# Optimization experiments

Hardware: AMD Instinct MI355X
Metric: run time of the kernel (lower is better)

Reference implementation:

```python
import jax, jax.numpy as jnp
import numpy as np

D_MODEL = 1024
D_INNER = 1024          # expand=1
NQK = 32
NV = 32
DSTATE = 64
DCONV = 4
CHUNK = 128
CONV_DIM = D_INNER + 2 * NQK * DSTATE          # 5120
HEADDIM = D_INNER // NV                         # 32
IN_PROJ_OUT = 2 * D_INNER + 2 * NQK * DSTATE + NV  # 6176


def setup_inputs() -> dict:
    key = jax.random.key(0)
    ks = jax.random.split(key, 6)
    B, L = 2, 8192
    u = jax.random.normal(ks[0], (B, L, D_MODEL), jnp.float32)
    W_in = jax.random.normal(ks[1], (IN_PROJ_OUT, D_MODEL), jnp.float32) * 0.02
    conv_w = jax.random.normal(ks[2], (CONV_DIM, DCONV), jnp.float32) * 0.2
    conv_b = jax.random.normal(ks[3], (CONV_DIM,), jnp.float32) * 0.02
    z_bias = jnp.zeros((D_INNER,), jnp.float32)
    D = jnp.ones((NV,), jnp.float32)
    W_out = jax.random.normal(ks[4], (D_MODEL, D_INNER), jnp.float32) * 0.02
    return {"u": u, "W_in": W_in, "conv_w": conv_w, "conv_b": conv_b,
            "z_bias": z_bias, "D": D, "W_out": W_out}


def _segsum(x):
    # x: (b,h,c,l) -> (b,h,c,l,l); entry (i,j) = sum_{j<s<=i} x_s for i>=j, masked else
    l = x.shape[-1]
    cs = jnp.cumsum(x, -1)
    seg = cs[..., :, None] - cs[..., None, :]
    mask = jnp.tril(jnp.ones((l, l), bool))
    return jnp.where(mask, seg, -1e9)


def reference(u, W_in, conv_w, conv_b, z_bias, D, W_out):
    b, L, _ = u.shape
    # in_proj and split: xBC | z | A_log
    xBCzA = u @ W_in.T
    xBC = xBCzA[..., :CONV_DIM]
    z = xBCzA[..., CONV_DIM:CONV_DIM + D_INNER]
    A_log = xBCzA[..., CONV_DIM + D_INNER:]          # (b,L,NV)
    # causal depthwise conv1d, identity activation
    xp = jnp.pad(xBC, ((0, 0), (DCONV - 1, 0), (0, 0)))
    xBC = sum(conv_w[:, k] * xp[:, k:k + L, :] for k in range(DCONV)) + conv_b
    # split x, B, C and reshape to heads
    x = xBC[..., :D_INNER].reshape(b, L, NV, HEADDIM)
    Bm = xBC[..., D_INNER:D_INNER + NQK * DSTATE].reshape(b, L, NQK, DSTATE)
    Cm = xBC[..., D_INNER + NQK * DSTATE:].reshape(b, L, NQK, DSTATE)
    # dt = softplus(A_log); A = -1 per head; kernel uses (x/dt) and multiplies dt back in
    dt = jax.nn.softplus(A_log)                      # (b,L,h)
    x_sc = x / dt[..., None]
    Xdt = x_sc * dt[..., None]
    Adt = -dt
    # chunked SSD (mamba_chunk_scan_combined math)
    nc = L // CHUNK
    Ac = Adt.reshape(b, nc, CHUNK, NV).transpose(0, 3, 1, 2)   # (b,h,c,l)
    A_cum = jnp.cumsum(Ac, -1)
    Lmat = jnp.exp(_segsum(Ac))                                # (b,h,c,l,l)
    Bc = Bm.reshape(b, nc, CHUNK, NQK, DSTATE)
    Cc = Cm.reshape(b, nc, CHUNK, NQK, DSTATE)
    Xc = Xdt.reshape(b, nc, CHUNK, NV, HEADDIM)
    # intra-chunk (diagonal block) output
    Y_diag = jnp.einsum('bclhn,bcshn,bhcls,bcshp->bclhp', Cc, Bc, Lmat, Xc)
    # per-chunk final states
    decay_states = jnp.exp(A_cum[..., -1:] - A_cum)            # (b,h,c,l)
    states = jnp.einsum('bclhn,bhcl,bclhp->bchpn', Bc, decay_states, Xc)
    dc = jnp.exp(A_cum[..., -1])                               # (b,h,c)
    st = jnp.moveaxis(states, 1, 0)                            # (c,b,h,p,n)
    dcs = jnp.moveaxis(dc, 2, 0)                               # (c,b,h)

    def step(S, inp):
        s_c, d_c = inp
        prev = S
        S = S * d_c[..., None, None] + s_c
        return S, prev

    S0 = jnp.zeros((b, NV, HEADDIM, DSTATE), Xdt.dtype)
    _, prevs = jax.lax.scan(step, S0, (st, dcs))               # (c,b,h,p,n)
    prevs = jnp.moveaxis(prevs, 0, 1)                          # (b,c,h,p,n)
    # inter-chunk (off-diagonal) contribution
    Y_off = jnp.einsum('bclhn,bchpn,bhcl->bclhp', Cc, prevs, jnp.exp(A_cum))
    y = (Y_diag + Y_off).reshape(b, L, NV, HEADDIM)
    # skip connection uses the UNscaled x (per torch code)
    y = y + D[None, None, :, None] * x
    y = y.reshape(b, L, D_INNER)
    # gated output projection
    return (y * jax.nn.silu(z + z_bias)) @ W_out.T
```

## Files before the change

### kernel.cpp

```cpp
#include <hip/hip_runtime.h>

typedef unsigned short u16;
typedef unsigned int   u32;
typedef __bf16  bf16x8 __attribute__((ext_vector_type(8)));
typedef float   f32x4  __attribute__((ext_vector_type(4)));
typedef unsigned int u32x4 __attribute__((ext_vector_type(4)));
typedef unsigned int u32x2 __attribute__((ext_vector_type(2)));

__device__ __forceinline__ float bf2f(u16 h){ return __uint_as_float(((u32)h)<<16); }
__device__ __forceinline__ u16 f2bf(float f){
  u32 u = __float_as_uint(f);
  u += 0x7FFFu + ((u>>16)&1u);
  return (u16)(u>>16);
}
__device__ __forceinline__ f32x4 mfma16(bf16x8 a, bf16x8 b, f32x4 c){
  return __builtin_amdgcn_mfma_f32_16x16x32_bf16(a,b,c,0,0,0);
}
__device__ __forceinline__ void ld16_lds(const u16* g, u16* l){
  __builtin_amdgcn_global_load_lds((const __attribute__((address_space(1))) u32*)g,
                                   (__attribute__((address_space(3))) u32*)l, 16, 0, 0);
}

__global__ __launch_bounds__(256) void cvt_kernel(const float* __restrict__ in,
                                                  u16* __restrict__ out, int n4){
  int i = blockIdx.x*256 + threadIdx.x;
  if (i < n4){
    float4 v = ((const float4*)in)[i];
    u32 p0 = (u32)f2bf(v.x) | ((u32)f2bf(v.y)<<16);
    u32 p1 = (u32)f2bf(v.z) | ((u32)f2bf(v.w)<<16);
    u32x2 pv = {p0, p1};
    *(u32x2*)(out + (size_t)i*4) = pv;
  }
}

__global__ __launch_bounds__(256) void dt_kernel(const float* __restrict__ u,
                                                 const float* __restrict__ Win,
                                                 float* __restrict__ dtb){
  __shared__ float us[8][1028];
  const int tid = threadIdx.x;
  const size_t t0 = (size_t)blockIdx.x*8;
  for (int i=tid; i<2048; i+=256){
    int row = i>>8, col = (i&255)*4;
    *(float4*)&us[row][col] = *(const float4*)(u + (t0+row)*1024 + col);
  }
  __syncthreads();
  const int tok = tid & 7, h = tid >> 3;
  const float* wp = Win + (size_t)(6144+h)*1024;
  float s0=0.f,s1=0.f,s2=0.f,s3=0.f;
  for (int k=0;k<1024;k+=4){
    float4 a  = *(const float4*)&us[tok][k];
    float4 wv = *(const float4*)&wp[k];
    s0 += a.x*wv.x; s1 += a.y*wv.y; s2 += a.z*wv.z; s3 += a.w*wv.w;
  }
  float s = (s0+s1)+(s2+s3);
  dtb[(t0+tok)*32 + h] = (s > 15.f) ? s : log1pf(expf(s));
}

__global__ __launch_bounds__(256,2) void gemm_in(const u16* __restrict__ A,
                                                 const u16* __restrict__ Bw,
                                                 u16* __restrict__ out0,
                                                 u16* __restrict__ out1,
                                                 const float* __restrict__ zb){
  __shared__ u16 As[128*32];
  __shared__ u16 Bs[128*32];
  const int tid  = threadIdx.x;
  const int lane = tid & 63;
  const int w = tid >> 6, wm = w >> 1, wn = w & 1;
  const int quad = lane >> 4, l15 = lane & 15;

  const int hwid = (int)(blockIdx.y*48 + blockIdx.x);
  const int tile = (hwid & 7)*384 + (hwid >> 3);
  const size_t m0 = (size_t)(tile / 48)*128, n0 = (size_t)(tile % 48)*128;

  f32x4 acc[4][4];
  #pragma unroll
  for (int i=0;i<4;i++)
    #pragma unroll
    for (int j=0;j<4;j++){ f32x4 z = {0.f,0.f,0.f,0.f}; acc[i][j] = z; }

  const int srow    = w*16 + (lane>>2);
  const int scol_sw = ((lane&3) ^ ((lane>>3)&3))*8;
  const u16* gA = A  + (m0+srow)*1024 + scol_sw;
  const u16* gB = Bw + (n0+srow)*1024 + scol_sw;
  u16* lA = As + w*512;
  u16* lB = Bs + w*512;

  const int swz = (quad*8) ^ (((l15>>1)&3)<<3);

  for (int k0 = 0; k0 < 1024; k0 += 32){
    __syncthreads();
    ld16_lds(gA,          lA);
    ld16_lds(gA + 64*1024, lA + 2048);
    ld16_lds(gB,          lB);
    ld16_lds(gB + 64*1024, lB + 2048);
    gA += 32; gB += 32;
    __syncthreads();
    bf16x8 av[4], bv[4];
    #pragma unroll
    for (int mi=0;mi<4;mi++) av[mi] = *(const bf16x8*)&As[(wm*64+mi*16+l15)*32 + swz];
    #pragma unroll
    for (int ni=0;ni<4;ni++) bv[ni] = *(const bf16x8*)&Bs[(wn*64+ni*16+l15)*32 + swz];
    #pragma unroll
    for (int mi=0;mi<4;mi++)
      #pragma unroll
      for (int ni=0;ni<4;ni++)
        acc[mi][ni] = mfma16(av[mi], bv[ni], acc[mi][ni]);
  }

  #pragma unroll
  for (int mi=0;mi<4;mi++){
    #pragma unroll
    for (int ni=0;ni<4;ni++){
      #pragma unroll
      for (int r=0;r<4;r++){
        size_t row = m0 + wm*64 + mi*16 + quad*4 + r;
        int    col = (int)n0 + wn*64 + ni*16 + l15;
        float v = acc[mi][ni][r];
        if (col < 5120){
          out0[row*5120 + col] = f2bf(v);
        } else {
          int ch = col - 5120;
          float z = v + zb[ch];
          float sg = z / (1.f + __expf(-z));
          out1[row*1024 + ch] = f2bf(sg);
        }
      }
    }
  }
}

__global__ __launch_bounds__(256,2) void gemm_out(const u16* __restrict__ A,
                                                  const u16* __restrict__ Bw,
                                                  float* __restrict__ out0){
  __shared__ u16 As[128*32];
  __shared__ u16 Bs[128*32];
  const int tid  = threadIdx.x;
  const int lane = tid & 63;
  const int w = tid >> 6, wm = w >> 1, wn = w & 1;
  const int quad = lane >> 4, l15 = lane & 15;

  const int hwid = (int)(blockIdx.y*8 + blockIdx.x);
  const int tile = (hwid & 7)*64 + (hwid >> 3);
  const size_t m0 = (size_t)(tile / 8)*128, n0 = (size_t)(tile % 8)*128;

  f32x4 acc[4][4];
  #pragma unroll
  for (int i=0;i<4;i++)
    #pragma unroll
    for (int j=0;j<4;j++){ f32x4 z = {0.f,0.f,0.f,0.f}; acc[i][j] = z; }

  const int srow    = w*16 + (lane>>2);
  const int scol_sw = ((lane&3) ^ ((lane>>3)&3))*8;
  const u16* gA = A  + (m0+srow)*1024 + scol_sw;
  const u16* gB = Bw + (n0+srow)*1024 + scol_sw;
  u16* lA = As + w*512;
  u16* lB = Bs + w*512;

  const int swz = (quad*8) ^ (((l15>>1)&3)<<3);

  for (int k0 = 0; k0 < 1024; k0 += 32){
    __syncthreads();
    ld16_lds(gA,          lA);
    ld16_lds(gA + 64*1024, lA + 2048);
    ld16_lds(gB,          lB);
    ld16_lds(gB + 64*1024, lB + 2048);
    gA += 32; gB += 32;
    __syncthreads();
    bf16x8 av[4], bv[4];
    #pragma unroll
    for (int mi=0;mi<4;mi++) av[mi] = *(const bf16x8*)&As[(wm*64+mi*16+l15)*32 + swz];
    #pragma unroll
    for (int ni=0;ni<4;ni++) bv[ni] = *(const bf16x8*)&Bs[(wn*64+ni*16+l15)*32 + swz];
    #pragma unroll
    for (int mi=0;mi<4;mi++)
      #pragma unroll
      for (int ni=0;ni<4;ni++)
        acc[mi][ni] = mfma16(av[mi], bv[ni], acc[mi][ni]);
  }

  #pragma unroll
  for (int mi=0;mi<4;mi++)
    #pragma unroll
    for (int ni=0;ni<4;ni++)
      #pragma unroll
      for (int r=0;r<4;r++){
        size_t row = m0 + wm*64 + mi*16 + quad*4 + r;
        int    col = (int)n0 + wn*64 + ni*16 + l15;
        out0[row*1024 + col] = acc[mi][ni][r];
      }
}

__global__ __launch_bounds__(256) void conv_kernel(const u16* __restrict__ xraw,
                                                   const float* __restrict__ cw,
                                                   const float* __restrict__ cb,
                                                   u16* __restrict__ xconv){
  const int c  = blockIdx.x*256 + threadIdx.x;
  const int t0 = blockIdx.y*8;
  const float w0=cw[c*4+0], w1=cw[c*4+1], w2=cw[c*4+2], w3=cw[c*4+3], bias=cb[c];
  const size_t base = (size_t)c;
  float h0 = (t0>=3) ? bf2f(xraw[base + (size_t)(t0-3)*5120]) : 0.f;
  float h1 = (t0>=2) ? bf2f(xraw[base + (size_t)(t0-2)*5120]) : 0.f;
  float h2 = (t0>=1) ? bf2f(xraw[base + (size_t)(t0-1)*5120]) : 0.f;
  #pragma unroll
  for (int i=0;i<8;i++){
    float x = bf2f(xraw[base + (size_t)(t0+i)*5120]);
    float o = w0*h0 + w1*h1 + w2*h2 + w3*x + bias;
    xconv[base + (size_t)(t0+i)*5120] = f2bf(o);
    h0=h1; h1=h2; h2=x;
  }
}

__global__ __launch_bounds__(256,1) void chunk1_kernel(const u16* __restrict__ xconv,
                                                       const float* __restrict__ dtb,
                                                       const float* __restrict__ Dvec,
                                                       float* __restrict__ ypart,
                                                       float* __restrict__ states,
                                                       float* __restrict__ dcb){
  __shared__ u16 Ps[128*136];
  __shared__ u16 XT[32*136];
  __shared__ u16 BT[64*136];
  __shared__ float Acum[128];
  __shared__ float decay[128];

  const int tid = threadIdx.x;
  const int lane = tid & 63;
  const int w = tid >> 6, quad = lane >> 4, l15 = lane & 15;
  const int blk = blockIdx.x;
  const int h = blk & 31, c = blk >> 5;
  const size_t tok0 = (size_t)c*128;
  const size_t xbase = tok0 * 5120;

  float mdt = 0.f;
  if (tid < 128) mdt = -dtb[(tok0 + tid)*32 + h];

  #pragma unroll
  for (int p=0;p<2;p++){
    int idx = p*256 + tid;
    int row = idx >> 2, col = (idx & 3)*8;
    u32x4 v = *(const u32x4*)(xconv + xbase + (size_t)row*5120 + h*32 + col);
    const u16* pv = (const u16*)&v;
    #pragma unroll
    for (int j=0;j<8;j++) XT[(col+j)*136 + row] = pv[j];
  }
  #pragma unroll
  for (int p=0;p<4;p++){
    int idx = p*256 + tid;
    int row = idx >> 3, col = (idx & 7)*8;
    u32x4 v = *(const u32x4*)(xconv + xbase + (size_t)row*5120 + 1024 + h*64 + col);
    const u16* pv = (const u16*)&v;
    #pragma unroll
    for (int j=0;j<8;j++) BT[(col+j)*136 + row] = pv[j];
  }
  if (tid < 128) Acum[tid] = mdt;
  __syncthreads();
  float run = mdt;
  for (int off=1; off<128; off<<=1){
    float add = 0.f;
    if (tid < 128 && tid >= off) add = Acum[tid-off];
    __syncthreads();
    if (tid < 128){ run += add; Acum[tid] = run; }
    __syncthreads();
  }
  float Alast = Acum[127];
  if (tid < 128) decay[tid] = __expf(Alast - Acum[tid]);
  if (tid == 0)  dcb[blk] = __expf(Alast);

  const int wm = w >> 1, wn = w & 1;
  f32x4 g[4][4];
  #pragma unroll
  for (int i=0;i<4;i++)
    #pragma unroll
    for (int j=0;j<4;j++){ f32x4 z = {0.f,0.f,0.f,0.f}; g[i][j] = z; }
  #pragma unroll
  for (int kk=0; kk<2; kk++){
    bf16x8 av[4], bv[4];
    #pragma unroll
    for (int mi=0;mi<4;mi++){
      int row = wm*64 + mi*16 + l15;
      av[mi] = *(const bf16x8*)(xconv + xbase + (size_t)row*5120 + 3072 + h*64 + kk*32 + quad*8);
    }
    #pragma unroll
    for (int ni=0;ni<4;ni++){
      int row = wn*64 + ni*16 + l15;
      bv[ni] = *(const bf16x8*)(xconv + xbase + (size_t)row*5120 + 1024 + h*64 + kk*32 + quad*8);
    }
    #pragma unroll
    for (int mi=0;mi<4;mi++)
      #pragma unroll
      for (int ni=0;ni<4;ni++)
        g[mi][ni] = mfma16(av[mi], bv[ni], g[mi][ni]);
  }
  #pragma unroll
  for (int mi=0;mi<4;mi++){
    int rowb = wm*64 + mi*16 + quad*4;
    #pragma unroll
    for (int ni=0;ni<4;ni++){
      int col = wn*64 + ni*16 + l15;
      float ac = Acum[col];
      #pragma unroll
      for (int r=0;r<4;r++){
        int row = rowb + r;
        float val = 0.f;
        if (col <= row) val = g[mi][ni][r] * __expf(Acum[row] - ac);
        Ps[row*136 + col] = f2bf(val);
      }
    }
  }
  __syncthreads();

  f32x4 yd[2][2];
  #pragma unroll
  for (int i=0;i<2;i++)
    #pragma unroll
    for (int j=0;j<2;j++){ f32x4 z = {0.f,0.f,0.f,0.f}; yd[i][j] = z; }
  #pragma unroll
  for (int kk=0;kk<4;kk++){
    bf16x8 av[2], bv[2];
    #pragma unroll
    for (int mi=0;mi<2;mi++) av[mi] = *(const bf16x8*)&Ps[(w*32+mi*16+l15)*136 + kk*32 + quad*8];
    #pragma unroll
    for (int ni=0;ni<2;ni++) bv[ni] = *(const bf16x8*)&XT[(ni*16+l15)*136 + kk*32 + quad*8];
    #pragma unroll
    for (int mi=0;mi<2;mi++)
      #pragma unroll
      for (int ni=0;ni<2;ni++)
        yd[mi][ni] = mfma16(av[mi], bv[ni], yd[mi][ni]);
  }
  float Dh = Dvec[h];
  #pragma unroll
  for (int mi=0;mi<2;mi++)
    #pragma unroll
    for (int ni=0;ni<2;ni++)
      #pragma unroll
      for (int r=0;r<4;r++){
        int row = w*32 + mi*16 + quad*4 + r;
        int col = ni*16 + l15;
        float xval = bf2f(XT[col*136 + row]);
        ypart[(tok0+row)*1024 + h*32 + col] = yd[mi][ni][r] + Dh*xval;
      }

  const int wm2 = w >> 1, wn2 = w & 1;
  f32x4 st[2];
  { f32x4 z = {0.f,0.f,0.f,0.f}; st[0]=z; st[1]=z; }
  #pragma unroll
  for (int kk=0;kk<4;kk++){
    bf16x8 av;
    {
      u32x4 xv = *(const u32x4*)&XT[(wm2*16+l15)*136 + kk*32 + quad*8];
      const u16* xp = (const u16*)&xv;
      #pragma unroll
      for (int j=0;j<8;j++) ((__bf16*)&av)[j] = (__bf16)(bf2f(xp[j]) * decay[kk*32 + quad*8 + j]);
    }
    bf16x8 bv[2];
    #pragma unroll
    for (int ni=0;ni<2;ni++) bv[ni] = *(const bf16x8*)&BT[(wn2*32+ni*16+l15)*136 + kk*32 + quad*8];
    #pragma unroll
    for (int ni=0;ni<2;ni++) st[ni] = mfma16(av, bv[ni], st[ni]);
  }
  size_t sbase = (size_t)blk * 2048;
  #pragma unroll
  for (int ni=0;ni<2;ni++)
    #pragma unroll
    for (int r=0;r<4;r++){
      int row = wm2*16 + quad*4 + r;
      int col = wn2*32 + ni*16 + l15;
      states[sbase + row*64 + col] = st[ni][r];
    }
}

__global__ __launch_bounds__(256) void scan_kernel(float* __restrict__ states,
                                                   const float* __restrict__ dcb){
  const int h = blockIdx.x >> 3;
  const int part = blockIdx.x & 7;
  const int pn = part*256 + threadIdx.x;
  float r[64];
  #pragma unroll
  for (int c=0;c<64;c++) r[c] = states[((size_t)(c*32 + h))*2048 + pn];
  float S = 0.f;
  #pragma unroll
  for (int c=0;c<64;c++){
    float stv = r[c];
    states[((size_t)(c*32 + h))*2048 + pn] = S;
    S = S*dcb[c*32 + h] + stv;
  }
}

__global__ __launch_bounds__(256,1) void chunk3_kernel(const u16* __restrict__ xconv,
                                                       const float* __restrict__ dtb,
                                                       const float* __restrict__ prevs,
                                                       const float* __restrict__ ypart,
                                                       const u16* __restrict__ gate,
                                                       u16* __restrict__ yg){
  __shared__ u16 Pv[32*72];
  __shared__ float Acum[128];
  const int tid = threadIdx.x;
  const int lane = tid & 63;
  const int w = tid >> 6, quad = lane >> 4, l15 = lane & 15;
  const int blk = blockIdx.x;
  const int h = blk & 31, c = blk >> 5;
  const size_t tok0 = (size_t)c*128;
  const size_t xbase = tok0 * 5120;

  float mdt = 0.f;
  if (tid < 128) mdt = -dtb[(tok0 + tid)*32 + h];
  size_t sbase = (size_t)blk * 2048;
  #pragma unroll
  for (int p=0;p<8;p++){
    int i = p*256 + tid;
    int pp = i >> 6, nn = i & 63;
    Pv[pp*72 + nn] = f2bf(prevs[sbase + i]);
  }
  if (tid < 128) Acum[tid] = mdt;
  __syncthreads();
  float run = mdt;
  for (int off=1; off<128; off<<=1){
    float add = 0.f;
    if (tid < 128 && tid >= off) add = Acum[tid-off];
    __syncthreads();
    if (tid < 128){ run += add; Acum[tid] = run; }
    __syncthreads();
  }

  f32x4 yo[2][2];
  #pragma unroll
  for (int i=0;i<2;i++)
    #pragma unroll
    for (int j=0;j<2;j++){ f32x4 z = {0.f,0.f,0.f,0.f}; yo[i][j] = z; }
  #pragma unroll
  for (int kk=0;kk<2;kk++){
    bf16x8 av[2], bv[2];
    #pragma unroll
    for (int mi=0;mi<2;mi++){
      int row = w*32 + mi*16 + l15;
      av[mi] = *(const bf16x8*)(xconv + xbase + (size_t)row*5120 + 3072 + h*64 + kk*32 + quad*8);
    }
    #pragma unroll
    for (int ni=0;ni<2;ni++) bv[ni] = *(const bf16x8*)&Pv[(ni*16+l15)*72 + kk*32 + quad*8];
    #pragma unroll
    for (int mi=0;mi<2;mi++)
      #pragma unroll
      for (int ni=0;ni<2;ni++)
        yo[mi][ni] = mfma16(av[mi], bv[ni], yo[mi][ni]);
  }
  #pragma unroll
  for (int mi=0;mi<2;mi++)
    #pragma unroll
    for (int ni=0;ni<2;ni++)
      #pragma unroll
      for (int r=0;r<4;r++){
        int row = w*32 + mi*16 + quad*4 + r;
        int col = ni*16 + l15;
        size_t gi = (tok0+row)*1024 + h*32 + col;
        float val = (ypart[gi] + __expf(Acum[row]) * yo[mi][ni][r]) * bf2f(gate[gi]);
        yg[gi] = f2bf(val);
      }
}

extern "C" void kernel_launch(void* const* d_in, const int* in_sizes, int n_in,
                              void* d_out, int out_size, void* d_ws, size_t ws_size,
                              hipStream_t stream){
  (void)out_size; (void)ws_size;
  static const int want[7] = {16777216, 6324224, 20480, 5120, 1024, 32, 1048576};
  const void* src[7] = {nullptr,nullptr,nullptr,nullptr,nullptr,nullptr,nullptr};
  if (n_in >= 7){
    for (int i=0;i<7;i++)
      for (int j=0;j<n_in;j++)
        if (in_sizes[j] == want[i]){ src[i] = d_in[j]; break; }
  }
  bool ok = true;
  for (int i=0;i<7;i++) if (!src[i]) ok = false;
  if (!ok) for (int i=0;i<7;i++) src[i] = d_in[i];
  const float* u      = (const float*)src[0];
  const float* W_in   = (const float*)src[1];
  const float* conv_w = (const float*)src[2];
  const float* conv_b = (const float*)src[3];
  const float* z_bias = (const float*)src[4];
  const float* Dvec   = (const float*)src[5];
  const float* W_out  = (const float*)src[6];
  float* out = (float*)d_out;

  char* p = (char*)d_ws;
  u16* wi_bf   = (u16*)p;   p += (size_t)6144*1024*2;
  u16* wo_bf   = (u16*)p;   p += (size_t)1024*1024*2;
  u16* u_bf    = (u16*)p;   p += (size_t)16384*1024*2;
  float* dtb   = (float*)p; p += (size_t)16384*32*4;
  float* dcb   = (float*)p; p += (size_t)4096*4;
  u16* gate    = (u16*)p;   p += (size_t)8192*1024*2;
  u16* yg      = (u16*)p;   p += (size_t)8192*1024*2;
  char* xbcA   = p;         p += (size_t)8192*5120*2;
  u16* xconv   = (u16*)p;   p += (size_t)8192*5120*2;

  u16*   xbc_raw = (u16*)xbcA;
  float* ypart   = (float*)xbcA;
  float* states  = (float*)(xbcA + (size_t)8192*1024*4);

  cvt_kernel<<<16384, 256, 0, stream>>>(u,     u_bf,  16384*1024/4);
  cvt_kernel<<<6144,  256, 0, stream>>>(W_in,  wi_bf, 6144*1024/4);
  cvt_kernel<<<1024,  256, 0, stream>>>(W_out, wo_bf, 1024*1024/4);
  dt_kernel<<<2048, 256, 0, stream>>>(u, W_in, dtb);

  for (int b = 0; b < 2; b++){
    const u16* ub_bf = u_bf + (size_t)b*8192*1024;
    float*     dtb_b = dtb  + (size_t)b*8192*32;
    float*     dcb_b = dcb  + (size_t)b*2048;
    float*     out_b = out  + (size_t)b*8192*1024;
    gemm_in<<<dim3(48,64), 256, 0, stream>>>(ub_bf, wi_bf, xbc_raw, gate, z_bias);
    conv_kernel<<<dim3(20,1024), 256, 0, stream>>>(xbc_raw, conv_w, conv_b, xconv);
    chunk1_kernel<<<2048, 256, 0, stream>>>(xconv, dtb_b, Dvec, ypart, states, dcb_b);
    scan_kernel<<<256, 256, 0, stream>>>(states, dcb_b);
    chunk3_kernel<<<2048, 256, 0, stream>>>(xconv, dtb_b, states, ypart, gate, yg);
    gemm_out<<<dim3(8,64), 256, 0, stream>>>(yg, wo_bf, out_b);
  }
}
```

Measured before the change: 807.6 us.

## Double-buffer LDS with BK=64 in input/output projection GEMMs

Both projection GEMMs now use a BK=64 K-tile with two LDS buffers, so global-to-LDS loads for the next tile are issued while MFMAs consume the current one. This halves the number of K iterations and removes one of the two barriers per step. The XOR swizzle changes to match 64-element rows, and the grouped tile-ordering remap is dropped in favour of direct blockIdx mapping. LDS use per block grows fourfold to 64 KB, which may limit the two-blocks-per-CU occupancy, and dropping the remap may hurt L2 reuse.

```diff
diff --git a/kernel.cpp b/kernel.cpp
--- a/kernel.cpp
+++ b/kernel.cpp
@@ -61,16 +61,13 @@
                                                  u16* __restrict__ out0,
                                                  u16* __restrict__ out1,
                                                  const float* __restrict__ zb){
-  __shared__ u16 As[128*32];
-  __shared__ u16 Bs[128*32];
+  __shared__ u16 As[2*128*64];
+  __shared__ u16 Bs[2*128*64];
   const int tid  = threadIdx.x;
   const int lane = tid & 63;
   const int w = tid >> 6, wm = w >> 1, wn = w & 1;
   const int quad = lane >> 4, l15 = lane & 15;
-
-  const int hwid = (int)(blockIdx.y*48 + blockIdx.x);
-  const int tile = (hwid & 7)*384 + (hwid >> 3);
-  const size_t m0 = (size_t)(tile / 48)*128, n0 = (size_t)(tile % 48)*128;
+  const size_t m0 = (size_t)blockIdx.y*128, n0 = (size_t)blockIdx.x*128;
 
   f32x4 acc[4][4];
   #pragma unroll
@@ -78,34 +75,64 @@
     #pragma unroll
     for (int j=0;j<4;j++){ f32x4 z = {0.f,0.f,0.f,0.f}; acc[i][j] = z; }
 
-  const int srow    = w*16 + (lane>>2);
-  const int scol_sw = ((lane&3) ^ ((lane>>3)&3))*8;
+  const int srow    = w*32 + (lane>>3);
+  const int scol_sw = ((lane&7) ^ (lane>>3))*8;
   const u16* gA = A  + (m0+srow)*1024 + scol_sw;
   const u16* gB = Bw + (n0+srow)*1024 + scol_sw;
-  u16* lA = As + w*512;
-  u16* lB = Bs + w*512;
-
-  const int swz = (quad*8) ^ (((l15>>1)&3)<<3);
-
-  for (int k0 = 0; k0 < 1024; k0 += 32){
-    __syncthreads();
-    ld16_lds(gA,          lA);
-    ld16_lds(gA + 64*1024, lA + 2048);
-    ld16_lds(gB,          lB);
-    ld16_lds(gB + 64*1024, lB + 2048);
-    gA += 32; gB += 32;
-    __syncthreads();
-    bf16x8 av[4], bv[4];
-    #pragma unroll
-    for (int mi=0;mi<4;mi++) av[mi] = *(const bf16x8*)&As[(wm*64+mi*16+l15)*32 + swz];
-    #pragma unroll
-    for (int ni=0;ni<4;ni++) bv[ni] = *(const bf16x8*)&Bs[(wn*64+ni*16+l15)*32 + swz];
-    #pragma unroll
-    for (int mi=0;mi<4;mi++)
-      #pragma unroll
-      for (int ni=0;ni<4;ni++)
-        acc[mi][ni] = mfma16(av[mi], bv[ni], acc[mi][ni]);
-  }
+  const int lofs = w*2048;
+
+#define STG(BUF) do{                                   \
+    u16* la = As + (BUF)*8192 + lofs;                  \
+    u16* lb = Bs + (BUF)*8192 + lofs;                  \
+    ld16_lds(gA,         la);                          \
+    ld16_lds(gA +  8192, la + 512);                    \
+    ld16_lds(gA + 16384, la + 1024);                   \
+    ld16_lds(gA + 24576, la + 1536);                   \
+    ld16_lds(gB,         lb);                          \
+    ld16_lds(gB +  8192, lb + 512);                    \
+    ld16_lds(gB + 16384, lb + 1024);                   \
+    ld16_lds(gB + 24576, lb + 1536);                   \
+    gA += 64; gB += 64; }while(0)
+
+#define CMP(BUF) do{                                                            \
+    _Pragma("unroll")                                                           \
+    for (int kk=0;kk<2;kk++){                                                   \
+      bf16x8 av[4], bv[4];                                                      \
+      _Pragma("unroll")                                                         \
+      for (int mi=0;mi<4;mi++){                                                 \
+        int row = wm*64+mi*16+l15;                                              \
+        av[mi] = *(const bf16x8*)&As[(BUF)*8192 + row*64 + (((kk*4+quad) ^ (l15&7))*8)]; \
+      }                                                                         \
+      _Pragma("unroll")                                                         \
+      for (int ni=0;ni<4;ni++){                                                 \
+        int row = wn*64+ni*16+l15;                                              \
+        bv[ni] = *(const bf16x8*)&Bs[(BUF)*8192 + row*64 + (((kk*4+quad) ^ (l15&7))*8)]; \
+      }                                                                         \
+      _Pragma("unroll")                                                         \
+      for (int mi=0;mi<4;mi++)                                                  \
+        _Pragma("unroll")                                                       \
+        for (int ni=0;ni<4;ni++)                                                \
+          acc[mi][ni] = mfma16(av[mi], bv[ni], acc[mi][ni]);                    \
+    } }while(0)
+
+  STG(0);
+  __syncthreads();
+  #pragma unroll 1
+  for (int t=0; t<14; t+=2){
+    STG(1);
+    CMP(0);
+    __syncthreads();
+    STG(0);
+    CMP(1);
+    __syncthreads();
+  }
+  STG(1);
+  CMP(0);
+  __syncthreads();
+  CMP(1);
+
+#undef STG
+#undef CMP
 
   #pragma unroll
   for (int mi=0;mi<4;mi++){
@@ -132,16 +159,13 @@
 __global__ __launch_bounds__(256,2) void gemm_out(const u16* __restrict__ A,
                                                   const u16* __restrict__ Bw,
                                                   float* __restrict__ out0){
-  __shared__ u16 As[128*32];
-  __shared__ u16 Bs[128*32];
+  __shared__ u16 As[2*128*64];
+  __shared__ u16 Bs[2*128*64];
   const int tid  = threadIdx.x;
   const int lane = tid & 63;
   const int w = tid >> 6, wm = w >> 1, wn = w & 1;
   const int quad = lane >> 4, l15 = lane & 15;
-
-  const int hwid = (int)(blockIdx.y*8 + blockIdx.x);
-  const int tile = (hwid & 7)*64 + (hwid >> 3);
-  const size_t m0 = (size_t)(tile / 8)*128, n0 = (size_t)(tile % 8)*128;
+  const size_t m0 = (size_t)blockIdx.y*128, n0 = (size_t)blockIdx.x*128;
 
   f32x4 acc[4][4];
   #pragma unroll
@@ -149,34 +173,64 @@
     #pragma unroll
     for (int j=0;j<4;j++){ f32x4 z = {0.f,0.f,0.f,0.f}; acc[i][j] = z; }
 
-  const int srow    = w*16 + (lane>>2);
-  const int scol_sw = ((lane&3) ^ ((lane>>3)&3))*8;
+  const int srow    = w*32 + (lane>>3);
+  const int scol_sw = ((lane&7) ^ (lane>>3))*8;
   const u16* gA = A  + (m0+srow)*1024 + scol_sw;
   const u16* gB = Bw + (n0+srow)*1024 + scol_sw;
-  u16* lA = As + w*512;
-  u16* lB = Bs + w*512;
-
-  const int swz = (quad*8) ^ (((l15>>1)&3)<<3);
-
-  for (int k0 = 0; k0 < 1024; k0 += 32){
-    __syncthreads();
-    ld16_lds(gA,          lA);
-    ld16_lds(gA + 64*1024, lA + 2048);
-    ld16_lds(gB,          lB);
-    ld16_lds(gB + 64*1024, lB + 2048);
-    gA += 32; gB += 32;
-    __syncthreads();
-    bf16x8 av[4], bv[4];
-    #pragma unroll
-    for (int mi=0;mi<4;mi++) av[mi] = *(const bf16x8*)&As[(wm*64+mi*16+l15)*32 + swz];
-    #pragma unroll
-    for (int ni=0;ni<4;ni++) bv[ni] = *(const bf16x8*)&Bs[(wn*64+ni*16+l15)*32 + swz];
-    #pragma unroll
-    for (int mi=0;mi<4;mi++)
-      #pragma unroll
-      for (int ni=0;ni<4;ni++)
-        acc[mi][ni] = mfma16(av[mi], bv[ni], acc[mi][ni]);
-  }
+  const int lofs = w*2048;
+
+#define STG(BUF) do{                                   \
+    u16* la = As + (BUF)*8192 + lofs;                  \
+    u16* lb = Bs + (BUF)*8192 + lofs;                  \
+    ld16_lds(gA,         la);                          \
+    ld16_lds(gA +  8192, la + 512);                    \
+    ld16_lds(gA + 16384, la + 1024);                   \
+    ld16_lds(gA + 24576, la + 1536);                   \
+    ld16_lds(gB,         lb);                          \
+    ld16_lds(gB +  8192, lb + 512);                    \
+    ld16_lds(gB + 16384, lb + 1024);                   \
+    ld16_lds(gB + 24576, lb + 1536);                   \
+    gA += 64; gB += 64; }while(0)
+
+#define CMP(BUF) do{                                                            \
+    _Pragma("unroll")                                                           \
+    for (int kk=0;kk<2;kk++){                                                   \
+      bf16x8 av[4], bv[4];                                                      \
+      _Pragma("unroll")                                                         \
+      for (int mi=0;mi<4;mi++){                                                 \
+        int row = wm*64+mi*16+l15;                                              \
+        av[mi] = *(const bf16x8*)&As[(BUF)*8192 + row*64 + (((kk*4+quad) ^ (l15&7))*8)]; \
+      }                                                                         \
+      _Pragma("unroll")                                                         \
+      for (int ni=0;ni<4;ni++){                                                 \
+        int row = wn*64+ni*16+l15;                                              \
+        bv[ni] = *(const bf16x8*)&Bs[(BUF)*8192 + row*64 + (((kk*4+quad) ^ (l15&7))*8)]; \
+      }                                                                         \
+      _Pragma("unroll")                                                         \
+      for (int mi=0;mi<4;mi++)                                                  \
+        _Pragma("unroll")                                                       \
+        for (int ni=0;ni<4;ni++)                                                \
+          acc[mi][ni] = mfma16(av[mi], bv[ni], acc[mi][ni]);                    \
+    } }while(0)
+
+  STG(0);
+  __syncthreads();
+  #pragma unroll 1
+  for (int t=0; t<14; t+=2){
+    STG(1);
+    CMP(0);
+    __syncthreads();
+    STG(0);
+    CMP(1);
+    __syncthreads();
+  }
+  STG(1);
+  CMP(0);
+  __syncthreads();
+  CMP(1);
+
+#undef STG
+#undef CMP
 
   #pragma unroll
   for (int mi=0;mi<4;mi++)
```

Result: slower. 845.4 us (+4.7%).
